# Optimization experiments

Measured on AMD Instinct MI355X. Metric: run time of the kernel, lower is better.

## Reference

```python
import jax, jax.numpy as jnp
import numpy as np

BETA = 0.9      # LIF leak
THRESH = 1.0    # snntorch Leaky default threshold
SLOPE = 25.0    # fast_sigmoid surrogate slope

@jax.custom_vjp
def spike(x):
    # Heaviside forward, fast_sigmoid surrogate backward
    return (x > 0).astype(x.dtype)

def _spike_fwd(x):
    return spike(x), x

def _spike_bwd(x, g):
    return (g / (SLOPE * jnp.abs(x) + 1.0) ** 2,)

spike.defvjp(_spike_fwd, _spike_bwd)


def setup_inputs() -> dict:
    key = jax.random.key(0)
    k0, k1, k2, k3, k4 = jax.random.split(key, 5)
    B, T, I, H, C = 256, 100, 512, 1024, 8
    x = jax.random.normal(k0, (B, T, I), dtype=jnp.float32)
    s1 = 1.0 / np.sqrt(I)
    s2 = 1.0 / np.sqrt(H)
    W1 = jax.random.uniform(k1, (H, I), jnp.float32, -s1, s1)
    b1 = jax.random.uniform(k2, (H,), jnp.float32, -s1, s1)
    W2 = jax.random.uniform(k3, (C, H), jnp.float32, -s2, s2)
    b2 = jax.random.uniform(k4, (C,), jnp.float32, -s2, s2)
    return {"x": x, "W1": W1, "b1": b1, "W2": W2, "b2": b2}


def reference(x, W1, b1, W2, b2):
    # x: [B, T, I]
    B, T, I = x.shape
    H = W1.shape[0]
    # fc1 for all timesteps as one big GEMM (same math as per-step loop).
    cur = jnp.einsum('bti,hi->tbh', x, W1) + b1  # [T, B, H]

    def step(mem, c):
        # snntorch Leaky (reset_mechanism='subtract'):
        reset = spike(mem - THRESH)
        mem_new = BETA * mem + c - reset * THRESH
        spk = spike(mem_new - THRESH)
        return mem_new, spk

    mem0 = jnp.zeros((B, H), dtype=x.dtype)
    _, spk_rec = jax.lax.scan(step, mem0, cur)  # spk_rec: [T, B, H]

    # sum_t (spk_t @ W2.T + b2) == (sum_t spk_t) @ W2.T + T*b2
    spk_sum = spk_rec.sum(axis=0)  # [B, H]
    logits = spk_sum @ W2.T + T * b2  # [B, C]
    return logits
```

## Files before the change

kernel.cpp:

```cpp
#include <hip/hip_runtime.h>


#define B_   256
#define T_   100
#define I_   512
#define H_   1024
#define C_   8
#define M_   (B_ * T_)
#define SC   64.0f
#define ISC  (1.0f / 4096.0f)

#define CELL_  512
#define SHALF_ 16384
#define PANEL_ 32768

typedef _Float16 half8 __attribute__((ext_vector_type(8)));
typedef float floatx16 __attribute__((ext_vector_type(16)));

__device__ __forceinline__ void ld_g2l(const _Float16* g, _Float16* l) {
    __builtin_amdgcn_global_load_lds(
        (const __attribute__((address_space(1))) void*)g,
        (__attribute__((address_space(3))) void*)l, 16, 0, 0);
}

__global__ void __launch_bounds__(256)
split_all(const float* __restrict__ x, const float* __restrict__ W1,
          const float* __restrict__ b2, _Float16* __restrict__ Asp,
          float* __restrict__ out) {
    const int tid = threadIdx.x;
    const int lane = tid & 63;
    const int w = tid >> 6;
    const int p = blockIdx.x;
    int g = p * 256 + tid;
    if (g < B_ * C_) out[g] = 100.0f * b2[g & (C_ - 1)];

    const bool isA = (p < 800);
    const int pl = isA ? p : (p - 800);
    const float* srcm = isA ? x : W1;
    _Float16* dstp = Asp + (size_t)(isA ? pl : (800 + pl)) * PANEL_;
#pragma unroll 2
    for (int j = 0; j < 8; ++j) {
        const int rl = j * 4 + w;
        const int r  = pl * 32 + rl;
        const float* src = srcm + (size_t)r * I_ + lane * 8;
        float4 v0 = *(const float4*)(src);
        float4 v1 = *(const float4*)(src + 4);
        float vv[8] = {v0.x, v0.y, v0.z, v0.w, v1.x, v1.y, v1.z, v1.w};
        half8 hi, lo;
#pragma unroll
        for (int q = 0; q < 8; ++q) {
            float s = vv[q] * SC;
            _Float16 h = (_Float16)s;
            hi[q] = h;
            lo[q] = (_Float16)(s - (float)h);
        }
        _Float16* d = dstp + (lane >> 1) * CELL_ + rl * 16 + (lane & 1) * 8;
        *(half8*)(d) = hi;
        *(half8*)(d + SHALF_) = lo;
    }
}

#define MFMA32(A, Bv, Cacc) \
    Cacc = __builtin_amdgcn_mfma_f32_32x32x16_f16(A, Bv, Cacc, 0, 0, 0)

__global__ void __launch_bounds__(256, 2)
snn_mfma(const _Float16* __restrict__ Asp, const _Float16* __restrict__ Wsp,
         const float* __restrict__ b1, const float* __restrict__ W2,
         float* __restrict__ logits) {
    __shared__ union {
        __align__(16) _Float16 buf[3][12288];
        float Cs[32 * 256];
    } sm;
    const int tid = threadIdx.x;
    const int lane = tid & 63;
    const int w = tid >> 6;

    const int xcd = blockIdx.x & 7;
    const int jj = blockIdx.x >> 3;
    const int b  = xcd * 32 + (jj >> 2);
    const int n0 = (jj & 3) * 256;

    const int wm = (w >> 1) * 64;
    const int wn = (w & 1) * 128;
    const int l31 = lane & 31;
    const int q2 = lane >> 5;

    const int lp = lane ^ ((lane >> 3) & 7);
    const int ra_row = b * T_ + w * 32 + (lp >> 1);
    const int rb_row = n0 + w * 64 + (lp >> 1);
    const _Float16* gah = Asp + (size_t)(ra_row >> 5) * PANEL_
                              + (ra_row & 31) * 16 + (lp & 1) * 8;
    const _Float16* gal = gah + SHALF_;
    const _Float16* gbh0 = Wsp + (size_t)(rb_row >> 5) * PANEL_
                               + (rb_row & 31) * 16 + (lp & 1) * 8;
    const _Float16* gbh1 = gbh0 + PANEL_;
    const _Float16* gbl0 = gbh0 + SHALF_;
    const _Float16* gbl1 = gbh1 + SHALF_;

    const int swz = ((l31 >> 2) & 7) << 3;
    const int ra = ((wm + l31) * 16 + q2 * 8) ^ swz;
    const int rb = ((wn + l31) * 16 + q2 * 8) ^ swz;

    floatx16 acc[2][4];
#pragma unroll
    for (int i = 0; i < 2; ++i)
#pragma unroll
        for (int j = 0; j < 4; ++j)
#pragma unroll
            for (int e = 0; e < 16; ++e) acc[i][j][e] = 0.f;

#pragma unroll
    for (int c0 = 0; c0 < 2; ++c0) {
        _Float16* nb = &sm.buf[0][0] + c0 * 12288;
        ld_g2l(gah  + c0 * CELL_, nb + w * 512);
        ld_g2l(gal  + c0 * CELL_, nb + 2048 + w * 512);
        ld_g2l(gbh0 + c0 * CELL_, nb + 4096 + w * 1024);
        ld_g2l(gbh1 + c0 * CELL_, nb + 4096 + w * 1024 + 512);
        ld_g2l(gbl0 + c0 * CELL_, nb + 8192 + w * 1024);
        ld_g2l(gbl1 + c0 * CELL_, nb + 8192 + w * 1024 + 512);
    }
    asm volatile("s_waitcnt vmcnt(6)" ::: "memory");
    __builtin_amdgcn_s_barrier();

    int bufc = 0, bufn = 2;
    for (int c = 0; c < 32; ++c) {
        const _Float16* bb = &sm.buf[0][0] + bufc * 12288;
        _Float16* nb = &sm.buf[0][0] + bufn * 12288;
        half8 ah[2], al[2], bh[2], bl[2];
        ah[0] = *(const half8*)(bb + ra);
        ah[1] = *(const half8*)(bb + ra + 512);
        al[0] = *(const half8*)(bb + 2048 + ra);
        al[1] = *(const half8*)(bb + 2048 + ra + 512);
        bh[0] = *(const half8*)(bb + 4096 + rb);
        bh[1] = *(const half8*)(bb + 4096 + rb + 512);
        bl[0] = *(const half8*)(bb + 8192 + rb);
        bl[1] = *(const half8*)(bb + 8192 + rb + 512);
        if (c < 30) {
            const int cc = c + 2;
            ld_g2l(gah  + cc * CELL_, nb + w * 512);
            ld_g2l(gal  + cc * CELL_, nb + 2048 + w * 512);
            ld_g2l(gbh0 + cc * CELL_, nb + 4096 + w * 1024);
        }
        __builtin_amdgcn_s_setprio(1);
        MFMA32(ah[0], bh[0], acc[0][0]); MFMA32(ah[0], bh[1], acc[0][1]);
        MFMA32(ah[1], bh[0], acc[1][0]); MFMA32(ah[1], bh[1], acc[1][1]);
        MFMA32(ah[0], bl[0], acc[0][0]); MFMA32(ah[0], bl[1], acc[0][1]);
        MFMA32(ah[1], bl[0], acc[1][0]); MFMA32(ah[1], bl[1], acc[1][1]);
        MFMA32(al[0], bh[0], acc[0][0]); MFMA32(al[0], bh[1], acc[0][1]);
        MFMA32(al[1], bh[0], acc[1][0]); MFMA32(al[1], bh[1], acc[1][1]);
        __builtin_amdgcn_s_setprio(0);
        __builtin_amdgcn_s_barrier();
        bh[0] = *(const half8*)(bb + 4096 + rb + 1024);
        bh[1] = *(const half8*)(bb + 4096 + rb + 1536);
        bl[0] = *(const half8*)(bb + 8192 + rb + 1024);
        bl[1] = *(const half8*)(bb + 8192 + rb + 1536);
        if (c < 30) {
            const int cc = c + 2;
            ld_g2l(gbh1 + cc * CELL_, nb + 4096 + w * 1024 + 512);
            ld_g2l(gbl0 + cc * CELL_, nb + 8192 + w * 1024);
            ld_g2l(gbl1 + cc * CELL_, nb + 8192 + w * 1024 + 512);
        }
        __builtin_amdgcn_s_setprio(1);
        MFMA32(ah[0], bh[0], acc[0][2]); MFMA32(ah[0], bh[1], acc[0][3]);
        MFMA32(ah[1], bh[0], acc[1][2]); MFMA32(ah[1], bh[1], acc[1][3]);
        MFMA32(ah[0], bl[0], acc[0][2]); MFMA32(ah[0], bl[1], acc[0][3]);
        MFMA32(ah[1], bl[0], acc[1][2]); MFMA32(ah[1], bl[1], acc[1][3]);
        MFMA32(al[0], bh[0], acc[0][2]); MFMA32(al[0], bh[1], acc[0][3]);
        MFMA32(al[1], bh[0], acc[1][2]); MFMA32(al[1], bh[1], acc[1][3]);
        __builtin_amdgcn_s_setprio(0);
        if (c < 30) {
            asm volatile("s_waitcnt vmcnt(6)" ::: "memory");
            __builtin_amdgcn_s_barrier();
        } else if (c == 30) {
            asm volatile("s_waitcnt vmcnt(0)" ::: "memory");
            __builtin_amdgcn_s_barrier();
        }
        bufc = (bufc == 2) ? 0 : bufc + 1;
        bufn = (bufn == 2) ? 0 : bufn + 1;
    }
    __syncthreads();

    float b1c[4];
#pragma unroll
    for (int fn = 0; fn < 4; ++fn) b1c[fn] = b1[n0 + wn + fn * 32 + l31];

    float mem = 0.f, ss = 0.f;

#pragma unroll
    for (int p = 0; p < 4; ++p) {
        const int fm = p & 1;
        if ((w >> 1) == (p >> 1)) {
#pragma unroll
            for (int r = 0; r < 16; ++r) {
                const int row = (r & 3) + 8 * (r >> 2) + 4 * q2;
                float* dst = &sm.Cs[row * 256 + wn + l31];
#pragma unroll
                for (int fn = 0; fn < 4; ++fn)
                    dst[fn * 32] = acc[fm][fn][r] * ISC + b1c[fn];
            }
        }
        __syncthreads();
        const int nt = (p == 3) ? 4 : 32;
#pragma unroll 8
        for (int t = 0; t < nt; ++t) {
            float cv = sm.Cs[t * 256 + tid];
            float reset = (mem > 1.0f) ? 1.0f : 0.0f;
            mem = 0.9f * mem + cv - reset;
            ss += (mem > 1.0f) ? 1.0f : 0.0f;
        }
        __syncthreads();
    }

#pragma unroll
    for (int cc = 0; cc < C_; ++cc) {
        float v = ss * W2[cc * H_ + n0 + tid];
#pragma unroll
        for (int off = 32; off; off >>= 1) v += __shfl_down(v, off, 64);
        if (lane == 0) atomicAdd(&logits[b * C_ + cc], v);
    }
}

extern "C" void kernel_launch(void* const* d_in, const int* in_sizes, int n_in,
                              void* d_out, int out_size, void* d_ws, size_t ws_size,
                              hipStream_t stream) {
    const float* x  = (const float*)d_in[0];
    const float* W1 = (const float*)d_in[1];
    const float* b1 = (const float*)d_in[2];
    const float* W2 = (const float*)d_in[3];
    const float* b2 = (const float*)d_in[4];
    float* out = (float*)d_out;

    char* ws = (char*)d_ws;
    _Float16* Asp = (_Float16*)ws;
    _Float16* Wsp = Asp + (size_t)800 * PANEL_;

    hipLaunchKernelGGL(split_all, dim3(832), dim3(256), 0, stream,
                       x, W1, b2, Asp, out);
    hipLaunchKernelGGL(snn_mfma, dim3(B_ * 4), dim3(256), 0, stream,
                       Asp, Wsp, b1, W2, out);
}
```

Baseline: 204.3 us.

## Fuse x fp16 hi/lo split into GEMM kernel, pre-split only W1

The separate pre-pass that converted all of x into scaled fp16 hi/lo panels is removed. The GEMM kernel now loads fp32 x rows directly into registers, splits them in-register one stage ahead, and writes the swizzled hi/lo halves to LDS. Only W1 is still pre-split, by a much smaller first kernel. This removes a full write and re-read of a ~100MB intermediate, at the cost of register-staged loads, extra VALU conversion work and LDS stores inside the pipelined main loop. Each of the four B_*4 column blocks now converts the same x rows, so that conversion work is duplicated per column block.

```diff
diff --git a/kernel.cpp b/kernel.cpp
--- a/kernel.cpp
+++ b/kernel.cpp
@@ -23,10 +23,21 @@
         (__attribute__((address_space(3))) void*)l, 16, 0, 0);
 }
 
+__device__ __forceinline__ void cvt_split(const float4 v0, const float4 v1,
+                                          half8& hi, half8& lo) {
+    float vv[8] = {v0.x, v0.y, v0.z, v0.w, v1.x, v1.y, v1.z, v1.w};
+#pragma unroll
+    for (int q = 0; q < 8; ++q) {
+        float s = vv[q] * SC;
+        _Float16 h = (_Float16)s;
+        hi[q] = h;
+        lo[q] = (_Float16)(s - (float)h);
+    }
+}
+
 __global__ void __launch_bounds__(256)
-split_all(const float* __restrict__ x, const float* __restrict__ W1,
-          const float* __restrict__ b2, _Float16* __restrict__ Asp,
-          float* __restrict__ out) {
+split_w1(const float* __restrict__ W1, const float* __restrict__ b2,
+         _Float16* __restrict__ Wsp, float* __restrict__ out) {
     const int tid = threadIdx.x;
     const int lane = tid & 63;
     const int w = tid >> 6;
@@ -34,26 +45,15 @@
     int g = p * 256 + tid;
     if (g < B_ * C_) out[g] = 100.0f * b2[g & (C_ - 1)];
 
-    const bool isA = (p < 800);
-    const int pl = isA ? p : (p - 800);
-    const float* srcm = isA ? x : W1;
-    _Float16* dstp = Asp + (size_t)(isA ? pl : (800 + pl)) * PANEL_;
+    _Float16* dstp = Wsp + (size_t)p * PANEL_;
 #pragma unroll 2
     for (int j = 0; j < 8; ++j) {
         const int rl = j * 4 + w;
-        const int r  = pl * 32 + rl;
-        const float* src = srcm + (size_t)r * I_ + lane * 8;
+        const float* src = W1 + (size_t)(p * 32 + rl) * I_ + lane * 8;
         float4 v0 = *(const float4*)(src);
         float4 v1 = *(const float4*)(src + 4);
-        float vv[8] = {v0.x, v0.y, v0.z, v0.w, v1.x, v1.y, v1.z, v1.w};
         half8 hi, lo;
-#pragma unroll
-        for (int q = 0; q < 8; ++q) {
-            float s = vv[q] * SC;
-            _Float16 h = (_Float16)s;
-            hi[q] = h;
-            lo[q] = (_Float16)(s - (float)h);
-        }
+        cvt_split(v0, v1, hi, lo);
         _Float16* d = dstp + (lane >> 1) * CELL_ + rl * 16 + (lane & 1) * 8;
         *(half8*)(d) = hi;
         *(half8*)(d + SHALF_) = lo;
@@ -64,7 +64,7 @@
     Cacc = __builtin_amdgcn_mfma_f32_32x32x16_f16(A, Bv, Cacc, 0, 0, 0)
 
 __global__ void __launch_bounds__(256, 2)
-snn_mfma(const _Float16* __restrict__ Asp, const _Float16* __restrict__ Wsp,
+snn_mfma(const float* __restrict__ x, const _Float16* __restrict__ Wsp,
          const float* __restrict__ b1, const float* __restrict__ W2,
          float* __restrict__ logits) {
     __shared__ union {
@@ -86,17 +86,19 @@
     const int q2 = lane >> 5;
 
     const int lp = lane ^ ((lane >> 3) & 7);
-    const int ra_row = b * T_ + w * 32 + (lp >> 1);
     const int rb_row = n0 + w * 64 + (lp >> 1);
-    const _Float16* gah = Asp + (size_t)(ra_row >> 5) * PANEL_
-                              + (ra_row & 31) * 16 + (lp & 1) * 8;
-    const _Float16* gal = gah + SHALF_;
     const _Float16* gbh0 = Wsp + (size_t)(rb_row >> 5) * PANEL_
                                + (rb_row & 31) * 16 + (lp & 1) * 8;
     const _Float16* gbh1 = gbh0 + PANEL_;
     const _Float16* gbl0 = gbh0 + SHALF_;
     const _Float16* gbl1 = gbh1 + SHALF_;
 
+    int rowm = b * T_ + w * 32 + (lane >> 1);
+    if (rowm > M_ - 1) rowm = M_ - 1;
+    const float* gxa = x + (size_t)rowm * I_ + (lane & 1) * 8;
+    const int wofs = (lane * 8) ^ (((lane >> 3) & 7) << 3) + 0;
+    _Float16* const abase = &sm.buf[0][0] + w * 512;
+
     const int swz = ((l31 >> 2) & 7) << 3;
     const int ra = ((wm + l31) * 16 + q2 * 8) ^ swz;
     const int rb = ((wn + l31) * 16 + q2 * 8) ^ swz;
@@ -109,23 +111,41 @@
 #pragma unroll
             for (int e = 0; e < 16; ++e) acc[i][j][e] = 0.f;
 
-#pragma unroll
-    for (int c0 = 0; c0 < 2; ++c0) {
-        _Float16* nb = &sm.buf[0][0] + c0 * 12288;
-        ld_g2l(gah  + c0 * CELL_, nb + w * 512);
-        ld_g2l(gal  + c0 * CELL_, nb + 2048 + w * 512);
-        ld_g2l(gbh0 + c0 * CELL_, nb + 4096 + w * 1024);
-        ld_g2l(gbh1 + c0 * CELL_, nb + 4096 + w * 1024 + 512);
-        ld_g2l(gbl0 + c0 * CELL_, nb + 8192 + w * 1024);
-        ld_g2l(gbl1 + c0 * CELL_, nb + 8192 + w * 1024 + 512);
-    }
-    asm volatile("s_waitcnt vmcnt(6)" ::: "memory");
-    __builtin_amdgcn_s_barrier();
-
-    int bufc = 0, bufn = 2;
+    float4 rxa0, rxb0, rxa1, rxb1;
+
+    {
+        _Float16* nb0 = &sm.buf[0][0];
+        _Float16* nb1 = &sm.buf[0][0] + 12288;
+        ld_g2l(gbh0, nb0 + 4096 + w * 1024);
+        ld_g2l(gbh1, nb0 + 4096 + w * 1024 + 512);
+        rxa0 = *(const float4*)(gxa);
+        rxb0 = *(const float4*)(gxa + 4);
+        ld_g2l(gbl0, nb0 + 8192 + w * 1024);
+        ld_g2l(gbl1, nb0 + 8192 + w * 1024 + 512);
+        ld_g2l(gbh0 + CELL_, nb1 + 4096 + w * 1024);
+        ld_g2l(gbh1 + CELL_, nb1 + 4096 + w * 1024 + 512);
+        rxa1 = *(const float4*)(gxa + 16);
+        rxb1 = *(const float4*)(gxa + 20);
+        ld_g2l(gbl0 + CELL_, nb1 + 8192 + w * 1024);
+        ld_g2l(gbl1 + CELL_, nb1 + 8192 + w * 1024 + 512);
+        asm volatile("s_waitcnt vmcnt(6)" ::: "memory");
+        half8 hi, lo;
+        cvt_split(rxa0, rxb0, hi, lo);
+        *(half8*)(abase + wofs) = hi;
+        *(half8*)(abase + 2048 + wofs) = lo;
+        asm volatile("s_waitcnt lgkmcnt(0)" ::: "memory");
+        __builtin_amdgcn_sched_barrier(0);
+        __builtin_amdgcn_s_barrier();
+        asm volatile("" ::: "memory");
+    }
+
+    int bufc = 0;
+#pragma unroll 2
     for (int c = 0; c < 32; ++c) {
+        const int bufn1 = (bufc == 2) ? 0 : bufc + 1;
+        const int bufn2 = (bufn1 == 2) ? 0 : bufn1 + 1;
         const _Float16* bb = &sm.buf[0][0] + bufc * 12288;
-        _Float16* nb = &sm.buf[0][0] + bufn * 12288;
+        _Float16* nb = &sm.buf[0][0] + bufn2 * 12288;
         half8 ah[2], al[2], bh[2], bl[2];
         ah[0] = *(const half8*)(bb + ra);
         ah[1] = *(const half8*)(bb + ra + 512);
@@ -136,10 +156,15 @@
         bl[0] = *(const half8*)(bb + 8192 + rb);
         bl[1] = *(const half8*)(bb + 8192 + rb + 512);
         if (c < 30) {
-            const int cc = c + 2;
-            ld_g2l(gah  + cc * CELL_, nb + w * 512);
-            ld_g2l(gal  + cc * CELL_, nb + 2048 + w * 512);
-            ld_g2l(gbh0 + cc * CELL_, nb + 4096 + w * 1024);
+            ld_g2l(gbh0 + (c + 2) * CELL_, nb + 4096 + w * 1024);
+            ld_g2l(gbh1 + (c + 2) * CELL_, nb + 4096 + w * 1024 + 512);
+            if ((c & 1) == 0) {
+                rxa0 = *(const float4*)(gxa + (c + 2) * 16);
+                rxb0 = *(const float4*)(gxa + (c + 2) * 16 + 4);
+            } else {
+                rxa1 = *(const float4*)(gxa + (c + 2) * 16);
+                rxb1 = *(const float4*)(gxa + (c + 2) * 16 + 4);
+            }
         }
         __builtin_amdgcn_s_setprio(1);
         MFMA32(ah[0], bh[0], acc[0][0]); MFMA32(ah[0], bh[1], acc[0][1]);
@@ -150,15 +175,14 @@
         MFMA32(al[1], bh[0], acc[1][0]); MFMA32(al[1], bh[1], acc[1][1]);
         __builtin_amdgcn_s_setprio(0);
         __builtin_amdgcn_s_barrier();
+        asm volatile("" ::: "memory");
         bh[0] = *(const half8*)(bb + 4096 + rb + 1024);
         bh[1] = *(const half8*)(bb + 4096 + rb + 1536);
         bl[0] = *(const half8*)(bb + 8192 + rb + 1024);
         bl[1] = *(const half8*)(bb + 8192 + rb + 1536);
         if (c < 30) {
-            const int cc = c + 2;
-            ld_g2l(gbh1 + cc * CELL_, nb + 4096 + w * 1024 + 512);
-            ld_g2l(gbl0 + cc * CELL_, nb + 8192 + w * 1024);
-            ld_g2l(gbl1 + cc * CELL_, nb + 8192 + w * 1024 + 512);
+            ld_g2l(gbl0 + (c + 2) * CELL_, nb + 8192 + w * 1024);
+            ld_g2l(gbl1 + (c + 2) * CELL_, nb + 8192 + w * 1024 + 512);
         }
         __builtin_amdgcn_s_setprio(1);
         MFMA32(ah[0], bh[0], acc[0][2]); MFMA32(ah[0], bh[1], acc[0][3]);
@@ -170,13 +194,22 @@
         __builtin_amdgcn_s_setprio(0);
         if (c < 30) {
             asm volatile("s_waitcnt vmcnt(6)" ::: "memory");
-            __builtin_amdgcn_s_barrier();
         } else if (c == 30) {
             asm volatile("s_waitcnt vmcnt(0)" ::: "memory");
-            __builtin_amdgcn_s_barrier();
-        }
-        bufc = (bufc == 2) ? 0 : bufc + 1;
-        bufn = (bufn == 2) ? 0 : bufn + 1;
+        }
+        if (c < 31) {
+            half8 hi, lo;
+            if ((c & 1) == 0) cvt_split(rxa1, rxb1, hi, lo);
+            else              cvt_split(rxa0, rxb0, hi, lo);
+            _Float16* ab = &sm.buf[0][0] + bufn1 * 12288 + w * 512;
+            *(half8*)(ab + wofs) = hi;
+            *(half8*)(ab + 2048 + wofs) = lo;
+            asm volatile("s_waitcnt lgkmcnt(0)" ::: "memory");
+            __builtin_amdgcn_sched_barrier(0);
+        }
+        __builtin_amdgcn_s_barrier();
+        asm volatile("" ::: "memory");
+        bufc = bufn1;
     }
     __syncthreads();
 
@@ -230,12 +263,10 @@
     const float* b2 = (const float*)d_in[4];
     float* out = (float*)d_out;
 
-    char* ws = (char*)d_ws;
-    _Float16* Asp = (_Float16*)ws;
-    _Float16* Wsp = Asp + (size_t)800 * PANEL_;
-
-    hipLaunchKernelGGL(split_all, dim3(832), dim3(256), 0, stream,
-                       x, W1, b2, Asp, out);
+    _Float16* Wsp = (_Float16*)d_ws;
+
+    hipLaunchKernelGGL(split_w1, dim3(32), dim3(256), 0, stream,
+                       W1, b2, Wsp, out);
     hipLaunchKernelGGL(snn_mfma, dim3(B_ * 4), dim3(256), 0, stream,
-                       Asp, Wsp, b1, W2, out);
-}
+                       x, Wsp, b1, W2, out);
+}
```

Measured after the change: 197.3 us. 3.4% less time.
